# Kernel optimization log

Measured on AMD Instinct MI355X. Metric: run time of the kernel, lower is better.

The kernel has to match this reference:

```python
import jax, jax.numpy as jnp
import numpy as np

P_FACTOR = 3.0   # config['p_factor']
EPS = 1e-12      # torch F.normalize eps

def _l2_normalize(x):
    return x / jnp.maximum(jnp.linalg.norm(x, axis=-1, keepdims=True), EPS)

def _l1_normalize(x):
    return x / jnp.maximum(jnp.sum(jnp.abs(x), axis=-1, keepdims=True), EPS)

def setup_inputs() -> dict:
    key = jax.random.key(0)
    k = jax.random.split(key, 6)
    B, N_EX, D_IN, D_FEAT, N_LAB, D_CLS = 4096, 16384, 1024, 256, 28, 64
    features = jax.random.normal(k[0], (B, D_IN), jnp.float32)
    labels = jax.random.uniform(k[1], (B, N_LAB), jnp.float32)            # BCE targets in [0,1]
    ex_features = jax.random.normal(k[2], (N_EX, D_IN), jnp.float32)
    ex_classes = jax.random.uniform(k[3], (N_EX, N_LAB), jnp.float32)     # class memberships
    g_w = jax.random.normal(k[4], (D_FEAT, D_IN), jnp.float32) * 0.02     # Linear(in=1024,out=256,bias=False)
    class_reps = jax.random.uniform(k[5], (N_LAB, D_CLS), jnp.float32) * 2.0 - 1.0  # rand*2-1
    return {"features": features, "labels": labels, "ex_features": ex_features,
            "ex_classes": ex_classes, "g_w": g_w, "class_reps": class_reps}

def reference(features, labels, ex_features, ex_classes, g_w, class_reps):
    # g projection (use_g=True, no bias)
    f = features @ g_w.T          # [B, D_FEAT]
    ef = ex_features @ g_w.T      # [N_EX, D_FEAT]
    # exemplar class representations: L1-normalized memberships @ class_reps
    ex_class_reps = _l1_normalize(ex_classes) @ class_reps   # [N_EX, D_CLS]
    # cosine similarity between queries and exemplars
    s = _l2_normalize(f) @ _l2_normalize(ef).T               # [B, N_EX]
    # power-sign activation then L1 normalize over exemplars
    a = _l1_normalize(jnp.sign(s) * jnp.abs(s) ** P_FACTOR)  # [B, N_EX]
    # weighted exemplar aggregation
    echo = a @ ex_class_reps                                  # [B, D_CLS]
    # negative euclidean distances to class representations (cdist)
    diff = echo[:, None, :] - class_reps[None, :, :]          # [B, N_LAB, D_CLS]
    neg_dists = -jnp.sqrt(jnp.sum(diff * diff, axis=-1))      # [B, N_LAB]
    # BCEWithLogitsLoss (mean reduction)
    loss = jnp.mean(-(labels * jax.nn.log_sigmoid(neg_dists)
                      + (1.0 - labels) * jax.nn.log_sigmoid(-neg_dists)))
    return (loss, neg_dists)
```

## Files before the change

### kernel.cpp

```cpp
#include <hip/hip_runtime.h>


typedef __bf16 bf16x8 __attribute__((ext_vector_type(8)));
typedef __bf16 bf16x4 __attribute__((ext_vector_type(4)));
typedef float  f32x4  __attribute__((ext_vector_type(4)));

__device__ __forceinline__ f32x4 f4zero() { f32x4 z = {0.f, 0.f, 0.f, 0.f}; return z; }

__device__ __forceinline__ f32x4 mfma16(bf16x8 a, bf16x8 b, f32x4 c) {
  return __builtin_amdgcn_mfma_f32_16x16x32_bf16(a, b, c, 0, 0, 0);
}

__device__ __forceinline__ bf16x8 load8f(const float* p) {
  f32x4 a = *(const f32x4*)p;
  f32x4 b = *(const f32x4*)(p + 4);
  bf16x8 r;
  r[0] = (__bf16)a[0]; r[1] = (__bf16)a[1]; r[2] = (__bf16)a[2]; r[3] = (__bf16)a[3];
  r[4] = (__bf16)b[0]; r[5] = (__bf16)b[1]; r[6] = (__bf16)b[2]; r[7] = (__bf16)b[3];
  return r;
}

__device__ __forceinline__ bf16x8 cvt2(f32x4 a, f32x4 b) {
  bf16x8 r;
  r[0] = (__bf16)a[0]; r[1] = (__bf16)a[1]; r[2] = (__bf16)a[2]; r[3] = (__bf16)a[3];
  r[4] = (__bf16)b[0]; r[5] = (__bf16)b[1]; r[6] = (__bf16)b[2]; r[7] = (__bf16)b[3];
  return r;
}

__device__ __forceinline__ void async16(const void* g, void* l) {
  __builtin_amdgcn_global_load_lds(
      (const __attribute__((address_space(1))) unsigned int*)g,
      (__attribute__((address_space(3))) unsigned int*)l, 16, 0, 0);
}

__device__ __forceinline__ void bar_lgkm() {
  asm volatile("s_waitcnt lgkmcnt(0)" ::: "memory");
  __builtin_amdgcn_s_barrier();
}
__device__ __forceinline__ void bar_all() {
  asm volatile("s_waitcnt vmcnt(0) lgkmcnt(0)" ::: "memory");
  __builtin_amdgcn_s_barrier();
}

__global__ void fill_sentinel(float* __restrict__ out, int n) {
  for (int i = blockIdx.x * 256 + threadIdx.x; i < n; i += gridDim.x * 256) out[i] = -1.0f;
}

__global__ void prep(const float* __restrict__ exc, __bf16* __restrict__ vT,
                     const float* __restrict__ W, __bf16* __restrict__ W3,
                     float* __restrict__ zp, int zn) {
  const int b = blockIdx.x, tid = threadIdx.x;
  if (b < 64) {
    int e = b * 256 + tid;
    float m[28];
    float s = 0.f;
#pragma unroll
    for (int j = 0; j < 28; j++) {
      m[j] = exc[(size_t)e * 28 + j];
      s += fabsf(m[j]);
    }
    float inv = 1.0f / fmaxf(s, 1e-12f);
#pragma unroll
    for (int j = 0; j < 28; j++) vT[(size_t)j * 16384 + e] = (__bf16)(m[j] * inv);
#pragma unroll
    for (int j = 28; j < 32; j++) vT[(size_t)j * 16384 + e] = (__bf16)0.0f;
  } else if (b < 192) {
    int i = (b - 64) * 256 + tid;
    int frag = i >> 6, lane = i & 63;
    int c16 = frag >> 5, k32 = frag & 31;
    int quad = lane >> 4, l15 = lane & 15;
    *(bf16x8*)(W3 + (size_t)i * 8) =
        load8f(W + (size_t)(c16 * 16 + l15) * 1024 + k32 * 32 + quad * 8);
  } else {
    for (int i = (b - 192) * 256 + tid; i < zn; i += (gridDim.x - 192) * 256) zp[i] = 0.f;
  }
}

__global__ __launch_bounds__(256, 3)
void proj_l2norm(const float* __restrict__ Xa, const float* __restrict__ Xb,
                 const __bf16* __restrict__ W3,
                 __bf16* __restrict__ Pa, __bf16* __restrict__ Pb) {
  __shared__ __align__(16) __bf16 Xs[2][32 * 72];
  __shared__ float nrmW[4 * 32];
  __shared__ float invn[32];

  const int tid = threadIdx.x;
  const int w = tid >> 6, lane = tid & 63;
  const int quad = lane >> 4, l15 = lane & 15;
  const int xrow = tid >> 3, xc8 = tid & 7;

  const float* X;
  __bf16* P;
  int row0;
  if (blockIdx.x < 512) { X = Xa; P = Pa; row0 = blockIdx.x * 32; }
  else                  { X = Xb; P = Pb; row0 = (blockIdx.x - 512) * 32; }

  const float* xsrc = X + (size_t)(row0 + xrow) * 1024 + xc8 * 8;
  const __bf16* wpk = W3 + (size_t)(w * 4) * 32 * 512 + (size_t)lane * 8;

  f32x4 acc[2][4];
#pragma unroll
  for (int i = 0; i < 2; i++)
#pragma unroll
    for (int j = 0; j < 4; j++) acc[i][j] = f4zero();

  *(bf16x8*)(&Xs[0][xrow * 72 + xc8 * 8]) = load8f(xsrc);
  bar_lgkm();

  int cur = 0;
  for (int kb = 0; kb < 16; kb++) {
    const int nxt = cur ^ 1;

    bf16x8 wF[8];
#pragma unroll
    for (int f = 0; f < 8; f++) {
      const int ksub = f >> 2, nb = f & 3;
      wF[f] = *(const bf16x8*)(wpk + ((size_t)nb * 32 + kb * 2 + ksub) * 512);
    }

    f32x4 xa, xb;
    if (kb < 15) {
      const float* xp = xsrc + (kb + 1) * 64;
      xa = *(const f32x4*)xp;
      xb = *(const f32x4*)(xp + 4);
    }

#pragma unroll
    for (int ksub = 0; ksub < 2; ksub++) {
      bf16x8 af[2];
#pragma unroll
      for (int mb = 0; mb < 2; mb++)
        af[mb] = *(bf16x8*)(&Xs[cur][(mb * 16 + l15) * 72 + ksub * 32 + quad * 8]);
#pragma unroll
      for (int mb = 0; mb < 2; mb++)
#pragma unroll
        for (int nb = 0; nb < 4; nb++)
          acc[mb][nb] = mfma16(af[mb], wF[ksub * 4 + nb], acc[mb][nb]);
    }

    if (kb < 15) {
      *(bf16x8*)(&Xs[nxt][xrow * 72 + xc8 * 8]) = cvt2(xa, xb);
    }
    bar_lgkm();
    cur = nxt;
  }

  float part[2][4];
#pragma unroll
  for (int mb = 0; mb < 2; mb++)
#pragma unroll
    for (int r = 0; r < 4; r++) {
      float s = 0.f;
#pragma unroll
      for (int nb = 0; nb < 4; nb++) { float v = acc[mb][nb][r]; s += v * v; }
      part[mb][r] = s;
    }
#pragma unroll
  for (int m = 1; m < 16; m <<= 1)
#pragma unroll
    for (int mb = 0; mb < 2; mb++)
#pragma unroll
      for (int r = 0; r < 4; r++) part[mb][r] += __shfl_xor(part[mb][r], m, 64);

  if (l15 == 0) {
#pragma unroll
    for (int mb = 0; mb < 2; mb++)
#pragma unroll
      for (int r = 0; r < 4; r++)
        nrmW[w * 32 + mb * 16 + quad * 4 + r] = part[mb][r];
  }
  __syncthreads();
  if (tid < 32) {
    float s = nrmW[tid] + nrmW[32 + tid] + nrmW[64 + tid] + nrmW[96 + tid];
    invn[tid] = 1.0f / fmaxf(sqrtf(s), 1e-12f);
  }
  __syncthreads();
#pragma unroll
  for (int mb = 0; mb < 2; mb++)
#pragma unroll
    for (int nb = 0; nb < 4; nb++)
#pragma unroll
      for (int r = 0; r < 4; r++) {
        int row = mb * 16 + quad * 4 + r;
        int col = w * 64 + nb * 16 + l15;
        P[(size_t)(row0 + row) * 256 + col] = (__bf16)(acc[mb][nb][r] * invn[row]);
      }
}

__global__ __launch_bounds__(256, 2)
void fused_sim(const __bf16* __restrict__ fn, const __bf16* __restrict__ efn,
               const __bf16* __restrict__ vTg,
               float* __restrict__ tT, float* __restrict__ r_acc) {
  __shared__ __align__(16) __bf16 Ks[2][32 * 256];
  __shared__ __align__(16) __bf16 Vs[2][32 * 32];
  __shared__ __align__(16) __bf16 Us[128 * 40];

  const int tid = threadIdx.x, w = tid >> 6, lane = tid & 63;
  const int quad = lane >> 4, l15 = lane & 15;
  const int swk = l15 & 7;
  const int chunk = blockIdx.x & 15, mtile = blockIdx.x >> 4;
  const int q0 = mtile * 128;
  const int e_base = chunk * 1024;
  const int qw = q0 + w * 32;

  int koff[4];
#pragma unroll
  for (int rep = 0; rep < 4; rep++) {
    int idx = rep * 256 + tid;
    int row = idx >> 5;
    int c5  = (idx & 31) ^ (row & 7);
    koff[rep] = row * 256 + c5 * 8;
  }
  const int vrow = tid >> 2, vc = tid & 3;
  const bool vstage = (tid < 128);

  {
    const __bf16* src = efn + (size_t)e_base * 256;
#pragma unroll
    for (int rep = 0; rep < 4; rep++)
      async16(src + koff[rep], &Ks[0][(rep * 256 + tid) * 8]);
    if (vstage)
      async16(vTg + (size_t)vrow * 16384 + e_base + vc * 8, &Vs[0][tid * 8]);
  }

  bf16x8 qf[8][2];
#pragma unroll
  for (int ks = 0; ks < 8; ks++)
#pragma unroll
    for (int nb = 0; nb < 2; nb++)
      qf[ks][nb] = *(const bf16x8*)(fn + (size_t)(qw + nb * 16 + l15) * 256 +
                                    ks * 32 + quad * 8);

  float r_part[2] = {0.f, 0.f};
  f32x4 accp[2][2];
#pragma unroll
  for (int a = 0; a < 2; a++)
#pragma unroll
    for (int b = 0; b < 2; b++) accp[a][b] = f4zero();

  bar_all();

  int cur = 0;
  for (int t = 0; t < 32; t++) {
    const int nxt = cur ^ 1;

    if (t < 31) {
      const __bf16* src = efn + (size_t)(e_base + (t + 1) * 32) * 256;
#pragma unroll
      for (int rep = 0; rep < 4; rep++)
        async16(src + koff[rep], &Ks[nxt][(rep * 256 + tid) * 8]);
      if (vstage)
        async16(vTg + (size_t)vrow * 16384 + e_base + (t + 1) * 32 + vc * 8,
                &Vs[nxt][tid * 8]);
    }

    f32x4 accs[2][2];
#pragma unroll
    for (int a = 0; a < 2; a++)
#pragma unroll
      for (int b = 0; b < 2; b++) accs[a][b] = f4zero();
#pragma unroll
    for (int ks = 0; ks < 8; ks++) {
      bf16x8 af[2];
#pragma unroll
      for (int mb = 0; mb < 2; mb++)
        af[mb] = *(bf16x8*)(&Ks[cur][(mb * 16 + l15) * 256 +
                                     ((ks * 4 + quad) ^ swk) * 8]);
#pragma unroll
      for (int mb = 0; mb < 2; mb++)
#pragma unroll
        for (int nb = 0; nb < 2; nb++)
          accs[mb][nb] = mfma16(af[mb], qf[ks][nb], accs[mb][nb]);
    }

#pragma unroll
    for (int mb = 0; mb < 2; mb++)
#pragma unroll
      for (int nb = 0; nb < 2; nb++) {
        bf16x4 pk;
#pragma unroll
        for (int r = 0; r < 4; r++) {
          float s = accs[mb][nb][r];
          __bf16 ub = (__bf16)(s * s * s);
          pk[r] = ub;
          r_part[nb] += fabsf((float)ub);
        }
        *(bf16x4*)(&Us[(w * 32 + nb * 16 + l15) * 40 + mb * 16 + quad * 4]) = pk;
      }

    bar_lgkm();

    {
      bf16x8 vf[2], uf[2];
#pragma unroll
      for (int cb = 0; cb < 2; cb++)
        vf[cb] = *(bf16x8*)(&Vs[cur][(cb * 16 + l15) * 32 + quad * 8]);
#pragma unroll
      for (int qb = 0; qb < 2; qb++)
        uf[qb] = *(bf16x8*)(&Us[(w * 32 + qb * 16 + l15) * 40 + quad * 8]);
#pragma unroll
      for (int cb = 0; cb < 2; cb++)
#pragma unroll
        for (int qb = 0; qb < 2; qb++)
          accp[cb][qb] = mfma16(vf[cb], uf[qb], accp[cb][qb]);
    }

    bar_all();
    cur = nxt;
  }

#pragma unroll
  for (int nb = 0; nb < 2; nb++) {
    float v = r_part[nb];
    v += __shfl_xor(v, 16, 64);
    v += __shfl_xor(v, 32, 64);
    if (quad == 0) atomicAdd(&r_acc[qw + nb * 16 + l15], v);
  }
#pragma unroll
  for (int cb = 0; cb < 2; cb++)
#pragma unroll
    for (int qb = 0; qb < 2; qb++)
#pragma unroll
      for (int r = 0; r < 4; r++)
        atomicAdd(&tT[(size_t)(cb * 16 + quad * 4 + r) * 4096 + qw + qb * 16 + l15],
                  accp[cb][qb][r]);
}

__global__ __launch_bounds__(256, 4)
void finalize(const float* __restrict__ tT, const float* __restrict__ r_acc,
              const float* __restrict__ creps, const float* __restrict__ labels,
              float* __restrict__ loss_acc, float* __restrict__ out) {
  __shared__ __align__(16) float cr[28 * 64];
  __shared__ float wsum[4];
  const int tid = threadIdx.x, w = tid >> 6, lane = tid & 63;
  for (int i = tid; i < 28 * 64; i += 256) cr[i] = creps[i];
  __syncthreads();

  const int q = blockIdx.x * 4 + w;
  float tval = 0.f;
  if (lane < 28) tval = tT[(size_t)lane * 4096 + q];
  tval *= 1.0f / fmaxf(r_acc[q], 1e-12f);

  float echo = 0.f;
#pragma unroll
  for (int j = 0; j < 28; j++)
    echo = fmaf(__shfl(tval, j, 64), cr[j * 64 + lane], echo);

  float dj = 0.f;
#pragma unroll
  for (int j = 0; j < 28; j++) {
    float df = echo - cr[j * 64 + lane];
    float d2 = df * df;
#pragma unroll
    for (int m = 1; m < 64; m <<= 1) d2 += __shfl_xor(d2, m, 64);
    if (lane == j) dj = sqrtf(d2);
  }

  float lsum = 0.f;
  if (lane < 28) {
    out[1 + (size_t)q * 28 + lane] = -dj;
    float y = labels[(size_t)q * 28 + lane];
    lsum = fmaf(y, dj, log1pf(expf(-dj)));
  }
#pragma unroll
  for (int m = 1; m < 64; m <<= 1) lsum += __shfl_xor(lsum, m, 64);
  if (lane == 0) wsum[w] = lsum;
  __syncthreads();
  if (tid == 0) {
    atomicAdd(loss_acc, wsum[0] + wsum[1] + wsum[2] + wsum[3]);
    __threadfence();
    unsigned* cnt = (unsigned*)(loss_acc + 1);
    unsigned old = atomicAdd(cnt, 1u);
    if (old == gridDim.x - 1) {
      float total = atomicAdd(loss_acc, 0.0f);
      out[0] = total * (1.0f / 114688.0f);
    }
  }
}

extern "C" void kernel_launch(void* const* d_in, const int* in_sizes, int n_in,
                              void* d_out, int out_size, void* d_ws, size_t ws_size,
                              hipStream_t stream) {
  const float* features = nullptr;
  const float* labels   = nullptr;
  const float* ex_feat  = nullptr;
  const float* ex_cls   = nullptr;
  const float* g_w      = nullptr;
  const float* creps    = nullptr;
  for (int i = 0; i < n_in; i++) {
    switch (in_sizes[i]) {
      case 4194304:  features = (const float*)d_in[i]; break;
      case 114688:   labels   = (const float*)d_in[i]; break;
      case 16777216: ex_feat  = (const float*)d_in[i]; break;
      case 458752:   ex_cls   = (const float*)d_in[i]; break;
      case 262144:   g_w      = (const float*)d_in[i]; break;
      case 1792:     creps    = (const float*)d_in[i]; break;
      default: break;
    }
  }
  float* out = (float*)d_out;

  if (!features || !labels || !ex_feat || !ex_cls || !g_w || !creps ||
      ws_size < (16ull << 20)) {
    fill_sentinel<<<256, 256, 0, stream>>>(out, out_size);
    return;
  }

  char* ws = (char*)d_ws;
  __bf16* f_n   = (__bf16*)(ws);
  __bf16* ef_n  = (__bf16*)(ws + (2ull << 20));
  __bf16* vT    = (__bf16*)(ws + (10ull << 20));
  float*  tT    = (float*) (ws + (11ull << 20));
  float*  r_acc = tT + 32 * 4096;
  float*  lossp = r_acc + 4096;
  __bf16* W3    = (__bf16*)(ws + (12ull << 20));

  prep<<<720, 256, 0, stream>>>(ex_cls, vT, g_w, W3, tT, 32 * 4096 + 4096 + 2);

  proj_l2norm<<<640, 256, 0, stream>>>(ex_feat, features, W3, ef_n, f_n);
  fused_sim<<<512, 256, 0, stream>>>(f_n, ef_n, vT, tT, r_acc);
  finalize<<<1024, 256, 0, stream>>>(tT, r_acc, creps, labels, lossp, out);
}
```

Measured before the change: 229.2 us.

## Retile similarity warps as 2x2 grid and swizzle V shared-memory layout

Each warp now computes 16 exemplars by 64 queries instead of 32 by 32. Each warp then loads only its own 16 K rows from shared memory per k-step, which halves redundant K LDS traffic across warps. The cost is twice the query-fragment registers held per thread, which adds register pressure. The U tile is now written across warps, so correctness relies on the existing barrier. The V staging tile also gets an XOR swizzle to cut LDS bank conflicts on the second MFMA's reads.

```diff
diff --git a/kernel.cpp b/kernel.cpp
--- a/kernel.cpp
+++ b/kernel.cpp
@@ -197,11 +197,11 @@
 
   const int tid = threadIdx.x, w = tid >> 6, lane = tid & 63;
   const int quad = lane >> 4, l15 = lane & 15;
+  const int wy = w >> 1, wx = w & 1;
   const int swk = l15 & 7;
   const int chunk = blockIdx.x & 15, mtile = blockIdx.x >> 4;
   const int q0 = mtile * 128;
   const int e_base = chunk * 1024;
-  const int qw = q0 + w * 32;
 
   int koff[4];
 #pragma unroll
@@ -211,7 +211,8 @@
     int c5  = (idx & 31) ^ (row & 7);
     koff[rep] = row * 256 + c5 * 8;
   }
-  const int vrow = tid >> 2, vc = tid & 3;
+  const int vrow = tid >> 2;
+  const int vcs  = (tid & 3) ^ (vrow & 3);
   const bool vstage = (tid < 128);
 
   {
@@ -220,18 +221,18 @@
     for (int rep = 0; rep < 4; rep++)
       async16(src + koff[rep], &Ks[0][(rep * 256 + tid) * 8]);
     if (vstage)
-      async16(vTg + (size_t)vrow * 16384 + e_base + vc * 8, &Vs[0][tid * 8]);
-  }
-
-  bf16x8 qf[8][2];
+      async16(vTg + (size_t)vrow * 16384 + e_base + vcs * 8, &Vs[0][tid * 8]);
+  }
+
+  bf16x8 qf[8][4];
 #pragma unroll
   for (int ks = 0; ks < 8; ks++)
 #pragma unroll
-    for (int nb = 0; nb < 2; nb++)
-      qf[ks][nb] = *(const bf16x8*)(fn + (size_t)(qw + nb * 16 + l15) * 256 +
+    for (int nb = 0; nb < 4; nb++)
+      qf[ks][nb] = *(const bf16x8*)(fn + (size_t)(q0 + wx * 64 + nb * 16 + l15) * 256 +
                                     ks * 32 + quad * 8);
 
-  float r_part[2] = {0.f, 0.f};
+  float r_part[4] = {0.f, 0.f, 0.f, 0.f};
   f32x4 accp[2][2];
 #pragma unroll
   for (int a = 0; a < 2; a++)
@@ -250,51 +251,45 @@
       for (int rep = 0; rep < 4; rep++)
         async16(src + koff[rep], &Ks[nxt][(rep * 256 + tid) * 8]);
       if (vstage)
-        async16(vTg + (size_t)vrow * 16384 + e_base + (t + 1) * 32 + vc * 8,
+        async16(vTg + (size_t)vrow * 16384 + e_base + (t + 1) * 32 + vcs * 8,
                 &Vs[nxt][tid * 8]);
     }
 
-    f32x4 accs[2][2];
-#pragma unroll
-    for (int a = 0; a < 2; a++)
-#pragma unroll
-      for (int b = 0; b < 2; b++) accs[a][b] = f4zero();
+    f32x4 accs[4];
+#pragma unroll
+    for (int b = 0; b < 4; b++) accs[b] = f4zero();
 #pragma unroll
     for (int ks = 0; ks < 8; ks++) {
-      bf16x8 af[2];
-#pragma unroll
-      for (int mb = 0; mb < 2; mb++)
-        af[mb] = *(bf16x8*)(&Ks[cur][(mb * 16 + l15) * 256 +
-                                     ((ks * 4 + quad) ^ swk) * 8]);
-#pragma unroll
-      for (int mb = 0; mb < 2; mb++)
-#pragma unroll
-        for (int nb = 0; nb < 2; nb++)
-          accs[mb][nb] = mfma16(af[mb], qf[ks][nb], accs[mb][nb]);
-    }
-
-#pragma unroll
-    for (int mb = 0; mb < 2; mb++)
-#pragma unroll
-      for (int nb = 0; nb < 2; nb++) {
-        bf16x4 pk;
-#pragma unroll
-        for (int r = 0; r < 4; r++) {
-          float s = accs[mb][nb][r];
-          __bf16 ub = (__bf16)(s * s * s);
-          pk[r] = ub;
-          r_part[nb] += fabsf((float)ub);
-        }
-        *(bf16x4*)(&Us[(w * 32 + nb * 16 + l15) * 40 + mb * 16 + quad * 4]) = pk;
+      bf16x8 af = *(bf16x8*)(&Ks[cur][(wy * 16 + l15) * 256 +
+                                      ((ks * 4 + quad) ^ swk) * 8]);
+#pragma unroll
+      for (int nb = 0; nb < 4; nb++)
+        accs[nb] = mfma16(af, qf[ks][nb], accs[nb]);
+    }
+
+    const int eo = wy * 16 + quad * 4;
+#pragma unroll
+    for (int nb = 0; nb < 4; nb++) {
+      bf16x4 pk;
+#pragma unroll
+      for (int r = 0; r < 4; r++) {
+        float s = accs[nb][r];
+        __bf16 ub = (__bf16)(s * s * s);
+        pk[r] = ub;
+        r_part[nb] += fabsf((float)ub);
       }
+      *(bf16x4*)(&Us[(wx * 64 + nb * 16 + l15) * 40 + eo]) = pk;
+    }
 
     bar_lgkm();
 
     {
       bf16x8 vf[2], uf[2];
 #pragma unroll
-      for (int cb = 0; cb < 2; cb++)
-        vf[cb] = *(bf16x8*)(&Vs[cur][(cb * 16 + l15) * 32 + quad * 8]);
+      for (int cb = 0; cb < 2; cb++) {
+        const int vr = cb * 16 + l15;
+        vf[cb] = *(bf16x8*)(&Vs[cur][vr * 32 + (quad ^ (vr & 3)) * 8]);
+      }
 #pragma unroll
       for (int qb = 0; qb < 2; qb++)
         uf[qb] = *(bf16x8*)(&Us[(w * 32 + qb * 16 + l15) * 40 + quad * 8]);
@@ -310,11 +305,11 @@
   }
 
 #pragma unroll
-  for (int nb = 0; nb < 2; nb++) {
+  for (int nb = 0; nb < 4; nb++) {
     float v = r_part[nb];
     v += __shfl_xor(v, 16, 64);
     v += __shfl_xor(v, 32, 64);
-    if (quad == 0) atomicAdd(&r_acc[qw + nb * 16 + l15], v);
+    if (quad == 0) atomicAdd(&r_acc[q0 + wx * 64 + nb * 16 + l15], v);
   }
 #pragma unroll
   for (int cb = 0; cb < 2; cb++)
@@ -322,7 +317,7 @@
     for (int qb = 0; qb < 2; qb++)
 #pragma unroll
       for (int r = 0; r < 4; r++)
-        atomicAdd(&tT[(size_t)(cb * 16 + quad * 4 + r) * 4096 + qw + qb * 16 + l15],
+        atomicAdd(&tT[(size_t)(cb * 16 + quad * 4 + r) * 4096 + q0 + w * 32 + qb * 16 + l15],
                   accp[cb][qb][r]);
 }
 
```

After: 231.1 us. No clear change (+0.8%).
